# Kernel tuning notes

Measured on AMD Instinct MI355X. Metric: run time of the kernel, lower is better.

The kernel has to match this reference:

```python
import jax, jax.numpy as jnp
import numpy as np

BLOCK = 64      # sparse block size (power of 2, >= 16)
NB = 128        # number of blocks -> max_seqlen = 8192
LOCAL = 8       # causal local window, in blocks
GLOBAL = 1      # leading global blocks every query attends to
K = LOCAL + GLOBAL
SM_SCALE = 1.0 / np.sqrt(64.0)  # default sm_scale = 1/sqrt(head_dim)


def _build_layout():
    # Fixed-width equivalent of the CSR block layout: for query block i,
    # live key blocks are the GLOBAL leading blocks plus the LOCAL-wide
    # causal window ending at i. Entries outside [0, i] are masked invalid;
    # global entries that fall inside the local window are invalidated to
    # avoid double counting.
    rows = np.arange(NB)[:, None]
    loc = rows - np.arange(LOCAL - 1, -1, -1)[None, :]      # [NB, LOCAL], ascending, ends at i
    glb = np.tile(np.arange(GLOBAL)[None, :], (NB, 1))      # [NB, GLOBAL]
    loc_valid = loc >= 0
    glb_valid = glb < (rows - LOCAL + 1)                    # strictly below local window
    col = np.concatenate([glb, np.maximum(loc, 0)], axis=1)  # [NB, K]
    valid = np.concatenate([glb_valid, loc_valid], axis=1)   # [NB, K]
    return col.astype(np.int32), valid


def setup_inputs() -> dict:
    key = jax.random.key(0)
    kq, kk, kv = jax.random.split(key, 3)
    B, S, H, D = 2, NB * BLOCK, 16, 64
    q = jax.random.normal(kq, (B, S, H, D), jnp.float32)
    k = jax.random.normal(kk, (B, S, H, D), jnp.float32)
    v = jax.random.normal(kv, (B, S, H, D), jnp.float32)
    col, valid = _build_layout()
    return {"q": q, "k": k, "v": v,
            "col_idx": jnp.asarray(col), "col_valid": jnp.asarray(valid)}


def reference(q, k, v, col_idx, col_valid):
    # Block-sparse causal attention. Only key/value blocks listed in
    # col_idx (where col_valid) are touched; token-level causal mask is
    # applied inside the gathered blocks (diagonal blocks get intra-block
    # causal masking, matching the kernel's behavior).
    B, S, H, D = q.shape
    bs = BLOCK
    nb = S // bs
    qb = q.reshape(B, nb, bs, H, D)                       # [B, nb, bs, H, D]
    kb = k.reshape(B, nb, bs, H, D)[:, col_idx]           # [B, nb, K, bs, H, D]
    vb = v.reshape(B, nb, bs, H, D)[:, col_idx]
    scores = jnp.einsum('bimhd,bijnhd->bhimjn', qb, kb) * SM_SCALE  # [B,H,nb,bs,K,bs]
    qpos = jnp.arange(nb)[:, None] * bs + jnp.arange(bs)[None, :]          # [nb, bs]
    kpos = col_idx[:, :, None] * bs + jnp.arange(bs)[None, None, :]        # [nb, K, bs]
    mask = (kpos[:, None, :, :] <= qpos[:, :, None, None]) & col_valid[:, None, :, None]
    neg = jnp.finfo(scores.dtype).min
    scores = jnp.where(mask[None, None], scores, neg)
    shp = scores.shape
    p = jax.nn.softmax(scores.reshape(shp[0], shp[1], shp[2], shp[3], -1), axis=-1).reshape(shp)
    out = jnp.einsum('bhimjn,bijnhd->bimhd', p, vb)       # [B, nb, bs, H, D]
    return out.reshape(B, S, H, D)
```

## Files before the change

kernel.cpp:

```cpp
#include <hip/hip_runtime.h>
#include <hip/hip_bf16.h>

#define NBQ     128
#define NLOCAL  8
#define NH      16
#define NBATCH  2
#define DIM     64
#define SEQ     (NBQ * 64)
#define QK_SCALE 0.1803368801111204f

typedef __attribute__((ext_vector_type(8))) short bf16x8;
typedef __attribute__((ext_vector_type(4))) short short4v;
typedef __attribute__((ext_vector_type(4))) float f32x4;
typedef __attribute__((ext_vector_type(2))) unsigned int u32x2;

__device__ inline short f2b(float x) {
    unsigned int u = __float_as_uint(x);
    return (short)((u + 0x8000u) >> 16);
}
__device__ inline unsigned int pack2(unsigned int lo_rnd, unsigned int hi_rnd) {
    return __builtin_amdgcn_perm(hi_rnd, lo_rnd, 0x07060302u);
}

typedef union { u32x2 u; short4v s; } pk_u;

__global__ __launch_bounds__(256, 3) void sparse_attn_kernel(
    const float* __restrict__ Q, const float* __restrict__ Kg,
    const float* __restrict__ Vg, float* __restrict__ Out)
{
    __shared__ __align__(16) short sK [2][64 * 64];
    __shared__ __align__(16) short sVt[2][64 * 64];

    const int gq  = blockIdx.x >> 5;
    const int bh  = blockIdx.x & 31;
    const int b   = bh >> 4;
    const int h   = bh & 15;
    const int qb0 = gq * 2, qb1 = qb0 + 1;
    const int tid  = threadIdx.x;
    const int wave = tid >> 6;
    const int lane = tid & 63;
    const int quad = lane >> 4;
    const int l15  = lane & 15;

    const int sg   = tid >> 4;
    const int t15c = tid & 15;
    const int tok4 = sg << 2;
    const int ft4  = t15c << 2;

    const int swk = l15 & 7;
    const int swv = ((l15 & 3) << 2) | ((l15 >> 2) & 3);

    bf16x8 qf0[2], qf1[2];
    {
        const int qrow = qb0 * 64 + wave * 16 + l15;
        const float* qp0 = Q + (((size_t)(b * SEQ + qrow)) * NH + h) * DIM;
        const float* qp1 = qp0 + (size_t)64 * NH * DIM;
#pragma unroll
        for (int ks = 0; ks < 2; ++ks) {
            const int o = ks * 32 + quad * 8;
            const f32x4 x0 = *(const f32x4*)(qp0 + o);
            const f32x4 x1 = *(const f32x4*)(qp0 + o + 4);
            const f32x4 y0 = *(const f32x4*)(qp1 + o);
            const f32x4 y1 = *(const f32x4*)(qp1 + o + 4);
            bf16x8 f, g;
#pragma unroll
            for (int c = 0; c < 4; ++c) {
                f[c]     = f2b(x0[c] * QK_SCALE);
                f[c + 4] = f2b(x1[c] * QK_SCALE);
                g[c]     = f2b(y0[c] * QK_SCALE);
                g[c + 4] = f2b(y1[c] * QK_SCALE);
            }
            qf0[ks] = f; qf1[ks] = g;
        }
    }

    float l0 = 0.f, l1 = 0.f;
    f32x4 o0[4], o1[4];
#pragma unroll
    for (int ft = 0; ft < 4; ++ft) { o0[ft] = (f32x4){0,0,0,0}; o1[ft] = (f32x4){0,0,0,0}; }

    const float* kbase = Kg + (size_t)b * (SEQ * NH * DIM);
    const float* vbase = Vg + (size_t)b * (SEQ * NH * DIM);
    const unsigned off0 = (unsigned)((tok4 * NH + h) * DIM + ft4);
    const int NHD = NH * DIM;

    const int lo    = (qb0 - 7 > 0) ? (qb0 - 7) : 0;
    const int has_g = (qb0 >= NLOCAL) ? 1 : 0;
    const int niter = (qb1 - lo + 1) + has_g;

    f32x4 kxr[4], vxr[4];
#pragma unroll
    for (int i = 0; i < 4; ++i) {
        kxr[i] = *(const f32x4*)(kbase + off0 + i * NHD);
        vxr[i] = *(const f32x4*)(vbase + off0 + i * NHD);
    }

    for (int it = 0; it < niter; ++it) {
        const int kb = (it < has_g) ? 0 : (lo + it - has_g);
        const int a0 = (kb == 0 && qb0 >= NLOCAL) || (kb >= qb0 - 7 && kb <= qb0);
        const int a1 = (kb == 0 && qb1 >= NLOCAL) || (kb >= qb1 - 7);
        short* sKb = &sK [it & 1][0];
        short* sVb = &sVt[it & 1][0];

        {
            unsigned int kr[4][4], vr[4][4];
#pragma unroll
            for (int i = 0; i < 4; ++i) {
#pragma unroll
                for (int c = 0; c < 4; ++c) {
                    kr[i][c] = __float_as_uint(kxr[i][c]) + 0x8000u;
                    vr[i][c] = __float_as_uint(vxr[i][c]) + 0x8000u;
                }
            }
#pragma unroll
            for (int i = 0; i < 4; ++i) {
                const int row  = tok4 + i;
                const int c16p = ((t15c >> 1) + (row & 7)) & 7;
                u32x2 w;
                w.x = pack2(kr[i][0], kr[i][1]);
                w.y = pack2(kr[i][2], kr[i][3]);
                *(u32x2*)&sKb[row * 64 + c16p * 8 + (t15c & 1) * 4] = w;
            }
#pragma unroll
            for (int c = 0; c < 4; ++c) {
                const int row = ft4 + c;
                const int sig = ((row & 3) << 2) | ((row >> 2) & 3);
                const int ch8 = (sg + sig) & 15;
                u32x2 w;
                w.x = pack2(vr[0][c], vr[1][c]);
                w.y = pack2(vr[2][c], vr[3][c]);
                *(u32x2*)&sVb[row * 64 + ch8 * 4] = w;
            }
        }

        __syncthreads();

        if (it + 1 < niter) {
            const int nkb = lo + (it + 1) - has_g;
            const unsigned nkoff = ((unsigned)nkb << 16) + off0;
#pragma unroll
            for (int i = 0; i < 4; ++i) {
                kxr[i] = *(const f32x4*)(kbase + nkoff + i * NHD);
                vxr[i] = *(const f32x4*)(vbase + nkoff + i * NHD);
            }
        }

        f32x4 s0[4], s1[4];
#pragma unroll
        for (int nt = 0; nt < 4; ++nt) {
            const int row = (nt * 16 + l15) * 64;
            const bf16x8 k0 = *(const bf16x8*)&sKb[row + (((quad     + swk) & 7) << 3)];
            const bf16x8 k1 = *(const bf16x8*)&sKb[row + (((4 + quad + swk) & 7) << 3)];
            f32x4 acc0 = (f32x4){0,0,0,0};
            acc0 = __builtin_amdgcn_mfma_f32_16x16x32_bf16(k0, qf0[0], acc0, 0, 0, 0);
            acc0 = __builtin_amdgcn_mfma_f32_16x16x32_bf16(k1, qf0[1], acc0, 0, 0, 0);
            s0[nt] = acc0;
            f32x4 acc1 = (f32x4){0,0,0,0};
            acc1 = __builtin_amdgcn_mfma_f32_16x16x32_bf16(k0, qf1[0], acc1, 0, 0, 0);
            acc1 = __builtin_amdgcn_mfma_f32_16x16x32_bf16(k1, qf1[1], acc1, 0, 0, 0);
            s1[nt] = acc1;
        }

        if (!a0) {
#pragma unroll
            for (int nt = 0; nt < 4; ++nt)
#pragma unroll
                for (int r = 0; r < 4; ++r) s0[nt][r] = -1e30f;
        } else if (kb == qb0) {
            const int qi = wave * 16 + l15;
#pragma unroll
            for (int nt = 0; nt < 4; ++nt)
#pragma unroll
                for (int r = 0; r < 4; ++r)
                    if (nt * 16 + quad * 4 + r > qi) s0[nt][r] = -1e30f;
        }
        if (!a1) {
#pragma unroll
            for (int nt = 0; nt < 4; ++nt)
#pragma unroll
                for (int r = 0; r < 4; ++r) s1[nt][r] = -1e30f;
        } else if (kb == qb1) {
            const int qi = wave * 16 + l15;
#pragma unroll
            for (int nt = 0; nt < 4; ++nt)
#pragma unroll
                for (int r = 0; r < 4; ++r)
                    if (nt * 16 + quad * 4 + r > qi) s1[nt][r] = -1e30f;
        }

        short4v pb0[4], pb1[4];
#pragma unroll
        for (int nt = 0; nt < 4; ++nt) {
            float ps0 = 0.f, ps1 = 0.f;
            unsigned int pr0[4], pr1[4];
#pragma unroll
            for (int r = 0; r < 4; ++r) {
                const float p0 = exp2f(s0[nt][r]);
                const float p1 = exp2f(s1[nt][r]);
                ps0 += p0; ps1 += p1;
                pr0[r] = __float_as_uint(p0) + 0x8000u;
                pr1[r] = __float_as_uint(p1) + 0x8000u;
            }
            l0 += ps0; l1 += ps1;
            pk_u pw0, pw1;
            pw0.u.x = pack2(pr0[0], pr0[1]); pw0.u.y = pack2(pr0[2], pr0[3]);
            pw1.u.x = pack2(pr1[0], pr1[1]); pw1.u.y = pack2(pr1[2], pr1[3]);
            pb0[nt] = pw0.s; pb1[nt] = pw1.s;
        }

#pragma unroll
        for (int ft = 0; ft < 4; ++ft) {
            const int row = (ft * 16 + l15) * 64;
#pragma unroll
            for (int nt = 0; nt < 4; ++nt) {
                const short4v va = *(const short4v*)&sVb[row + (((nt * 4 + quad + swv) & 15) << 2)];
                o0[ft] = __builtin_amdgcn_mfma_f32_16x16x16bf16_1k(va, pb0[nt], o0[ft], 0, 0, 0);
                o1[ft] = __builtin_amdgcn_mfma_f32_16x16x16bf16_1k(va, pb1[nt], o1[ft], 0, 0, 0);
            }
        }
    }

    l0 += __shfl_xor(l0, 16); l0 += __shfl_xor(l0, 32);
    l1 += __shfl_xor(l1, 16); l1 += __shfl_xor(l1, 32);
    const float inv0 = 1.0f / l0;
    const float inv1 = 1.0f / l1;
    const int qrow = qb0 * 64 + wave * 16 + l15;
    float* op0 = Out + (((size_t)(b * SEQ + qrow)) * NH + h) * DIM + quad * 4;
    float* op1 = op0 + (size_t)64 * NH * DIM;
#pragma unroll
    for (int ft = 0; ft < 4; ++ft) {
        *(f32x4*)(op0 + ft * 16) = o0[ft] * inv0;
        *(f32x4*)(op1 + ft * 16) = o1[ft] * inv1;
    }
}

extern "C" void kernel_launch(void* const* d_in, const int* in_sizes, int n_in,
                              void* d_out, int out_size, void* d_ws, size_t ws_size,
                              hipStream_t stream) {
    const float* q = (const float*)d_in[0];
    const float* k = (const float*)d_in[1];
    const float* v = (const float*)d_in[2];
    float* out = (float*)d_out;
    dim3 grid((NBQ / 2) * NBATCH * NH);
    sparse_attn_kernel<<<grid, dim3(256), 0, stream>>>(q, k, v, out);
}
```

Baseline: 280.2 us.

## Process key/value blocks in pairs with one barrier per pair

Replaces the one-tile-ahead register prefetch loop with a loop that issues global loads for two K/V blocks at once. It converts and stages both into the two LDS buffers, synchronises once, then computes both tiles. This halves the number of block-wide barriers and doubles the loads in flight per wave. In exchange, loads are no longer overlapped with the previous tile's MFMA compute, and holding two tiles in registers raises VGPR pressure.

```diff
diff --git a/kernel.cpp b/kernel.cpp
--- a/kernel.cpp
+++ b/kernel.cpp
@@ -88,62 +88,40 @@
     const int has_g = (qb0 >= NLOCAL) ? 1 : 0;
     const int niter = (qb1 - lo + 1) + has_g;
 
-    f32x4 kxr[4], vxr[4];
-#pragma unroll
-    for (int i = 0; i < 4; ++i) {
-        kxr[i] = *(const f32x4*)(kbase + off0 + i * NHD);
-        vxr[i] = *(const f32x4*)(vbase + off0 + i * NHD);
-    }
-
-    for (int it = 0; it < niter; ++it) {
-        const int kb = (it < has_g) ? 0 : (lo + it - has_g);
+    auto stage_tile = [&](const f32x4 kx[4], const f32x4 vx[4], short* sKb, short* sVb) {
+        unsigned int kr[4][4], vr[4][4];
+#pragma unroll
+        for (int i = 0; i < 4; ++i) {
+#pragma unroll
+            for (int c = 0; c < 4; ++c) {
+                kr[i][c] = __float_as_uint(kx[i][c]) + 0x8000u;
+                vr[i][c] = __float_as_uint(vx[i][c]) + 0x8000u;
+            }
+        }
+#pragma unroll
+        for (int i = 0; i < 4; ++i) {
+            const int row  = tok4 + i;
+            const int c16p = ((t15c >> 1) + (row & 7)) & 7;
+            u32x2 w;
+            w.x = pack2(kr[i][0], kr[i][1]);
+            w.y = pack2(kr[i][2], kr[i][3]);
+            *(u32x2*)&sKb[row * 64 + c16p * 8 + (t15c & 1) * 4] = w;
+        }
+#pragma unroll
+        for (int c = 0; c < 4; ++c) {
+            const int row = ft4 + c;
+            const int sig = ((row & 3) << 2) | ((row >> 2) & 3);
+            const int ch8 = (sg + sig) & 15;
+            u32x2 w;
+            w.x = pack2(vr[0][c], vr[1][c]);
+            w.y = pack2(vr[2][c], vr[3][c]);
+            *(u32x2*)&sVb[row * 64 + ch8 * 4] = w;
+        }
+    };
+
+    auto compute_tile = [&](const int kb, const short* sKb, const short* sVb) {
         const int a0 = (kb == 0 && qb0 >= NLOCAL) || (kb >= qb0 - 7 && kb <= qb0);
         const int a1 = (kb == 0 && qb1 >= NLOCAL) || (kb >= qb1 - 7);
-        short* sKb = &sK [it & 1][0];
-        short* sVb = &sVt[it & 1][0];
-
-        {
-            unsigned int kr[4][4], vr[4][4];
-#pragma unroll
-            for (int i = 0; i < 4; ++i) {
-#pragma unroll
-                for (int c = 0; c < 4; ++c) {
-                    kr[i][c] = __float_as_uint(kxr[i][c]) + 0x8000u;
-                    vr[i][c] = __float_as_uint(vxr[i][c]) + 0x8000u;
-                }
-            }
-#pragma unroll
-            for (int i = 0; i < 4; ++i) {
-                const int row  = tok4 + i;
-                const int c16p = ((t15c >> 1) + (row & 7)) & 7;
-                u32x2 w;
-                w.x = pack2(kr[i][0], kr[i][1]);
-                w.y = pack2(kr[i][2], kr[i][3]);
-                *(u32x2*)&sKb[row * 64 + c16p * 8 + (t15c & 1) * 4] = w;
-            }
-#pragma unroll
-            for (int c = 0; c < 4; ++c) {
-                const int row = ft4 + c;
-                const int sig = ((row & 3) << 2) | ((row >> 2) & 3);
-                const int ch8 = (sg + sig) & 15;
-                u32x2 w;
-                w.x = pack2(vr[0][c], vr[1][c]);
-                w.y = pack2(vr[2][c], vr[3][c]);
-                *(u32x2*)&sVb[row * 64 + ch8 * 4] = w;
-            }
-        }
-
-        __syncthreads();
-
-        if (it + 1 < niter) {
-            const int nkb = lo + (it + 1) - has_g;
-            const unsigned nkoff = ((unsigned)nkb << 16) + off0;
-#pragma unroll
-            for (int i = 0; i < 4; ++i) {
-                kxr[i] = *(const f32x4*)(kbase + nkoff + i * NHD);
-                vxr[i] = *(const f32x4*)(vbase + nkoff + i * NHD);
-            }
-        }
 
         f32x4 s0[4], s1[4];
 #pragma unroll
@@ -218,6 +196,41 @@
                 o1[ft] = __builtin_amdgcn_mfma_f32_16x16x16bf16_1k(va, pb1[nt], o1[ft], 0, 0, 0);
             }
         }
+    };
+
+    for (int it = 0; it < niter; it += 2) {
+        const int kb0i  = (it < has_g) ? 0 : (lo + it - has_g);
+        const bool have2 = (it + 1 < niter);
+        const int kb1i  = lo + (it + 1) - has_g;
+
+        f32x4 k0x[4], v0x[4], k1x[4], v1x[4];
+        {
+            const unsigned koff0 = ((unsigned)kb0i << 16) + off0;
+#pragma unroll
+            for (int i = 0; i < 4; ++i) {
+                k0x[i] = *(const f32x4*)(kbase + koff0 + i * NHD);
+                v0x[i] = *(const f32x4*)(vbase + koff0 + i * NHD);
+            }
+        }
+        if (have2) {
+            const unsigned koff1 = ((unsigned)kb1i << 16) + off0;
+#pragma unroll
+            for (int i = 0; i < 4; ++i) {
+                k1x[i] = *(const f32x4*)(kbase + koff1 + i * NHD);
+                v1x[i] = *(const f32x4*)(vbase + koff1 + i * NHD);
+            }
+        }
+        __builtin_amdgcn_sched_barrier(0);
+
+        stage_tile(k0x, v0x, &sK[0][0], &sVt[0][0]);
+        if (have2) stage_tile(k1x, v1x, &sK[1][0], &sVt[1][0]);
+
+        __syncthreads();
+
+        compute_tile(kb0i, &sK[0][0], &sVt[0][0]);
+        if (have2) compute_tile(kb1i, &sK[1][0], &sVt[1][0]);
+
+        if (it + 2 < niter) __syncthreads();
     }
 
     l0 += __shfl_xor(l0, 16); l0 += __shfl_xor(l0, 32);
```

Measured after the change: 256.1 us. -8.6%, faster.

## Single-buffer LDS with inline-asm loads, explicit waits, and hardware bf16 pack

Applied to the files above, without the earlier changes.

Replaces the double-buffered K/V shared memory with a single buffer guarded by two barriers per iteration, which halves LDS use and may allow higher occupancy. Global loads are issued through inline asm with an explicit vmcnt wait, so the compiler cannot insert or reorder the waits. fp32-to-bf16 conversion now uses the hardware v_cvt_pk_bf16_f32 instruction instead of add-and-perm rounding. The extra barrier adds synchronisation cost, and the conversion now rounds to nearest even rather than rounding half up.

```diff
diff --git a/kernel.cpp b/kernel.cpp
--- a/kernel.cpp
+++ b/kernel.cpp
@@ -18,18 +18,35 @@
     unsigned int u = __float_as_uint(x);
     return (short)((u + 0x8000u) >> 16);
 }
-__device__ inline unsigned int pack2(unsigned int lo_rnd, unsigned int hi_rnd) {
-    return __builtin_amdgcn_perm(hi_rnd, lo_rnd, 0x07060302u);
+__device__ inline unsigned int cvtpk(float lo, float hi) {
+    unsigned int r;
+    asm("v_cvt_pk_bf16_f32 %0, %1, %2" : "=v"(r) : "v"(lo), "v"(hi));
+    return r;
 }
 
 typedef union { u32x2 u; short4v s; } pk_u;
+
+__device__ inline void gload(f32x4& dst, const float* p) {
+    asm volatile("global_load_dwordx4 %0, %1, off" : "=v"(dst) : "v"(p));
+}
+__device__ inline void wait_vm0(f32x4& a0, f32x4& a1, f32x4& a2, f32x4& a3,
+                                f32x4& b0, f32x4& b1, f32x4& b2, f32x4& b3) {
+    asm volatile("s_waitcnt vmcnt(0)"
+                 : "+v"(a0), "+v"(a1), "+v"(a2), "+v"(a3),
+                   "+v"(b0), "+v"(b1), "+v"(b2), "+v"(b3));
+}
+__device__ inline void lds_barrier() {
+    asm volatile("s_waitcnt lgkmcnt(0)" ::: "memory");
+    __builtin_amdgcn_s_barrier();
+    asm volatile("" ::: "memory");
+}
 
 __global__ __launch_bounds__(256, 3) void sparse_attn_kernel(
     const float* __restrict__ Q, const float* __restrict__ Kg,
     const float* __restrict__ Vg, float* __restrict__ Out)
 {
-    __shared__ __align__(16) short sK [2][64 * 64];
-    __shared__ __align__(16) short sVt[2][64 * 64];
+    __shared__ __align__(16) short sK [64 * 64];
+    __shared__ __align__(16) short sVt[64 * 64];
 
     const int gq  = blockIdx.x >> 5;
     const int bh  = blockIdx.x & 31;
@@ -91,66 +108,57 @@
     f32x4 kxr[4], vxr[4];
 #pragma unroll
     for (int i = 0; i < 4; ++i) {
-        kxr[i] = *(const f32x4*)(kbase + off0 + i * NHD);
-        vxr[i] = *(const f32x4*)(vbase + off0 + i * NHD);
+        gload(kxr[i], kbase + off0 + i * NHD);
+        gload(vxr[i], vbase + off0 + i * NHD);
     }
 
     for (int it = 0; it < niter; ++it) {
         const int kb = (it < has_g) ? 0 : (lo + it - has_g);
         const int a0 = (kb == 0 && qb0 >= NLOCAL) || (kb >= qb0 - 7 && kb <= qb0);
         const int a1 = (kb == 0 && qb1 >= NLOCAL) || (kb >= qb1 - 7);
-        short* sKb = &sK [it & 1][0];
-        short* sVb = &sVt[it & 1][0];
-
-        {
-            unsigned int kr[4][4], vr[4][4];
-#pragma unroll
-            for (int i = 0; i < 4; ++i) {
-#pragma unroll
-                for (int c = 0; c < 4; ++c) {
-                    kr[i][c] = __float_as_uint(kxr[i][c]) + 0x8000u;
-                    vr[i][c] = __float_as_uint(vxr[i][c]) + 0x8000u;
-                }
-            }
-#pragma unroll
-            for (int i = 0; i < 4; ++i) {
-                const int row  = tok4 + i;
-                const int c16p = ((t15c >> 1) + (row & 7)) & 7;
-                u32x2 w;
-                w.x = pack2(kr[i][0], kr[i][1]);
-                w.y = pack2(kr[i][2], kr[i][3]);
-                *(u32x2*)&sKb[row * 64 + c16p * 8 + (t15c & 1) * 4] = w;
-            }
-#pragma unroll
-            for (int c = 0; c < 4; ++c) {
-                const int row = ft4 + c;
-                const int sig = ((row & 3) << 2) | ((row >> 2) & 3);
-                const int ch8 = (sg + sig) & 15;
-                u32x2 w;
-                w.x = pack2(vr[0][c], vr[1][c]);
-                w.y = pack2(vr[2][c], vr[3][c]);
-                *(u32x2*)&sVb[row * 64 + ch8 * 4] = w;
-            }
-        }
-
-        __syncthreads();
+
+        wait_vm0(kxr[0], kxr[1], kxr[2], kxr[3], vxr[0], vxr[1], vxr[2], vxr[3]);
+
+        lds_barrier();
+
+#pragma unroll
+        for (int i = 0; i < 4; ++i) {
+            const int row  = tok4 + i;
+            const int c16p = ((t15c >> 1) + (row & 7)) & 7;
+            u32x2 w;
+            w.x = cvtpk(kxr[i][0], kxr[i][1]);
+            w.y = cvtpk(kxr[i][2], kxr[i][3]);
+            *(u32x2*)&sK[row * 64 + c16p * 8 + (t15c & 1) * 4] = w;
+        }
+#pragma unroll
+        for (int c = 0; c < 4; ++c) {
+            const int row = ft4 + c;
+            const int sig = ((row & 3) << 2) | ((row >> 2) & 3);
+            const int ch8 = (sg + sig) & 15;
+            u32x2 w;
+            w.x = cvtpk(vxr[0][c], vxr[1][c]);
+            w.y = cvtpk(vxr[2][c], vxr[3][c]);
+            *(u32x2*)&sVt[row * 64 + ch8 * 4] = w;
+        }
 
         if (it + 1 < niter) {
             const int nkb = lo + (it + 1) - has_g;
             const unsigned nkoff = ((unsigned)nkb << 16) + off0;
 #pragma unroll
             for (int i = 0; i < 4; ++i) {
-                kxr[i] = *(const f32x4*)(kbase + nkoff + i * NHD);
-                vxr[i] = *(const f32x4*)(vbase + nkoff + i * NHD);
-            }
-        }
+                gload(kxr[i], kbase + nkoff + i * NHD);
+                gload(vxr[i], vbase + nkoff + i * NHD);
+            }
+        }
+
+        lds_barrier();
 
         f32x4 s0[4], s1[4];
 #pragma unroll
         for (int nt = 0; nt < 4; ++nt) {
             const int row = (nt * 16 + l15) * 64;
-            const bf16x8 k0 = *(const bf16x8*)&sKb[row + (((quad     + swk) & 7) << 3)];
-            const bf16x8 k1 = *(const bf16x8*)&sKb[row + (((4 + quad + swk) & 7) << 3)];
+            const bf16x8 k0 = *(const bf16x8*)&sK[row + (((quad     + swk) & 7) << 3)];
+            const bf16x8 k1 = *(const bf16x8*)&sK[row + (((4 + quad + swk) & 7) << 3)];
             f32x4 acc0 = (f32x4){0,0,0,0};
             acc0 = __builtin_amdgcn_mfma_f32_16x16x32_bf16(k0, qf0[0], acc0, 0, 0, 0);
             acc0 = __builtin_amdgcn_mfma_f32_16x16x32_bf16(k1, qf0[1], acc0, 0, 0, 0);
@@ -192,19 +200,17 @@
 #pragma unroll
         for (int nt = 0; nt < 4; ++nt) {
             float ps0 = 0.f, ps1 = 0.f;
-            unsigned int pr0[4], pr1[4];
+            float p0[4], p1[4];
 #pragma unroll
             for (int r = 0; r < 4; ++r) {
-                const float p0 = exp2f(s0[nt][r]);
-                const float p1 = exp2f(s1[nt][r]);
-                ps0 += p0; ps1 += p1;
-                pr0[r] = __float_as_uint(p0) + 0x8000u;
-                pr1[r] = __float_as_uint(p1) + 0x8000u;
+                p0[r] = exp2f(s0[nt][r]);
+                p1[r] = exp2f(s1[nt][r]);
+                ps0 += p0[r]; ps1 += p1[r];
             }
             l0 += ps0; l1 += ps1;
             pk_u pw0, pw1;
-            pw0.u.x = pack2(pr0[0], pr0[1]); pw0.u.y = pack2(pr0[2], pr0[3]);
-            pw1.u.x = pack2(pr1[0], pr1[1]); pw1.u.y = pack2(pr1[2], pr1[3]);
+            pw0.u.x = cvtpk(p0[0], p0[1]); pw0.u.y = cvtpk(p0[2], p0[3]);
+            pw1.u.x = cvtpk(p1[0], p1[1]); pw1.u.y = cvtpk(p1[2], p1[3]);
             pb0[nt] = pw0.s; pb1[nt] = pw1.s;
         }
 
@@ -213,7 +219,7 @@
             const int row = (ft * 16 + l15) * 64;
 #pragma unroll
             for (int nt = 0; nt < 4; ++nt) {
-                const short4v va = *(const short4v*)&sVb[row + (((nt * 4 + quad + swv) & 15) << 2)];
+                const short4v va = *(const short4v*)&sVt[row + (((nt * 4 + quad + swv) & 15) << 2)];
                 o0[ft] = __builtin_amdgcn_mfma_f32_16x16x16bf16_1k(va, pb0[nt], o0[ft], 0, 0, 0);
                 o1[ft] = __builtin_amdgcn_mfma_f32_16x16x16bf16_1k(va, pb1[nt], o1[ft], 0, 0, 0);
             }
```

Result: faster. 247.4 us (-11.7%).
